# Performance work log

Measured on AMD Instinct MI355X. Metric: run time of the kernel, lower is better.

Reference implementation:

```python
import jax, jax.numpy as jnp
import numpy as np

N_SLOTS = 256
CHANNELS = 2048

def setup_inputs() -> dict:
    key = jax.random.key(0)
    k1, k2, k3, k4 = jax.random.split(key, 4)
    B, C, H, W = 32, CHANNELS, 32, 32
    x = jax.random.normal(k1, (B, C, H, W), dtype=jnp.float32)
    slot_assign = jax.random.randint(k2, (B, H, W), 0, N_SLOTS, dtype=jnp.int32)
    # slot noise tables: alpha ~ N(1, sigma1), beta ~ N(0, sigma2)
    sigma1, sigma2 = 0.1, 0.1
    alpha = 1.0 + sigma1 * jax.random.normal(k3, (N_SLOTS, CHANNELS), dtype=jnp.float32)
    beta = sigma2 * jax.random.normal(k4, (N_SLOTS, CHANNELS), dtype=jnp.float32)
    return {"x": x, "slot_assign": slot_assign, "alpha": alpha, "beta": beta}

def reference(x, slot_assign, alpha, beta):
    # Gather per-pixel (alpha, beta) rows: [B,H,W,C] -> move C to axis 1
    a = jnp.transpose(alpha[slot_assign], (0, 3, 1, 2))  # [B,C,H,W]
    b = jnp.transpose(beta[slot_assign], (0, 3, 1, 2))   # [B,C,H,W]
    return a * x + b
```

## Files before the change

### kernel.cpp

```cpp
#include <hip/hip_runtime.h>


typedef float  f4 __attribute__((ext_vector_type(4)));
typedef int    i4 __attribute__((ext_vector_type(4)));

#define CH   2048
#define HW   1024
#define NS   256
#define CPB  8
#define NCG  (CH / CPB)
#define IPB  4

__global__ __launch_bounds__(256, 4) void fa_kernel(
    const float* __restrict__ x,
    const int*   __restrict__ slot,
    const float* __restrict__ alpha,
    const float* __restrict__ beta,
    float*       __restrict__ out)
{
    __shared__ float lds_a[CPB][NS];
    __shared__ float lds_b[CPB][NS];

    const int cg = blockIdx.x & (NCG - 1);
    const int bg = blockIdx.x >> 8;
    const int b0 = bg * IPB;
    const int c0 = cg * CPB;
    const int t  = threadIdx.x;
    const int p  = t << 2;

    const f4 ar0 = *(const f4*)(alpha + (size_t)t * CH + c0);
    const f4 ar1 = *(const f4*)(alpha + (size_t)t * CH + c0 + 4);
    const f4 br0 = *(const f4*)(beta  + (size_t)t * CH + c0);
    const f4 br1 = *(const f4*)(beta  + (size_t)t * CH + c0 + 4);

#pragma unroll
    for (int k = 0; k < 4; ++k) {
        lds_a[k][t]     = ar0[k];
        lds_a[4 + k][t] = ar1[k];
        lds_b[k][t]     = br0[k];
        lds_b[4 + k][t] = br1[k];
    }

    __syncthreads();

#pragma unroll
    for (int i = 0; i < IPB; ++i) {
        const int b = b0 + i;

        const i4 s = *(const i4*)(slot + (size_t)b * HW + p);

        const size_t base = ((size_t)b * CH + c0) * HW + p;
        f4 xv[CPB];
#pragma unroll
        for (int k = 0; k < CPB; ++k)
            xv[k] = __builtin_nontemporal_load((const f4*)(x + base + (size_t)k * HW));

#pragma unroll
        for (int k = 0; k < CPB; ++k) {
            const float a0 = lds_a[k][s.x], a1 = lds_a[k][s.y],
                        a2 = lds_a[k][s.z], a3 = lds_a[k][s.w];
            const float b0v = lds_b[k][s.x], b1v = lds_b[k][s.y],
                        b2v = lds_b[k][s.z], b3v = lds_b[k][s.w];
            f4 o;
            o[0] = a0 * xv[k][0] + b0v;
            o[1] = a1 * xv[k][1] + b1v;
            o[2] = a2 * xv[k][2] + b2v;
            o[3] = a3 * xv[k][3] + b3v;
            __builtin_nontemporal_store(o, (f4*)(out + base + (size_t)k * HW));
        }
    }
}

extern "C" void kernel_launch(void* const* d_in, const int* in_sizes, int n_in,
                              void* d_out, int out_size, void* d_ws, size_t ws_size,
                              hipStream_t stream) {
    const float* x     = (const float*)d_in[0];
    const int*   slot  = (const int*)d_in[1];
    const float* alpha = (const float*)d_in[2];
    const float* beta  = (const float*)d_in[3];
    float*       out   = (float*)d_out;

    const int B = in_sizes[0] / (CH * HW);
    dim3 grid((B / IPB) * NCG);
    dim3 block(256);
    fa_kernel<<<grid, block, 0, stream>>>(x, slot, alpha, beta, out);
}
```

Before: 429.6 us.

## Double-buffer x and slot loads across images and double images per block

The kernel now prefetches the next image's slot indices and x tile into registers while the current image is being computed. The first image's loads are issued before the LDS table fill and barrier. Images per block go from 4 to 8, halving the grid and amortizing the alpha/beta table load over more work. The cost is higher register pressure from two x buffers, which could limit occupancy under launch_bounds(256,4), and fewer blocks to fill the device.

```diff
diff --git a/kernel.cpp b/kernel.cpp
--- a/kernel.cpp
+++ b/kernel.cpp
@@ -9,7 +9,7 @@
 #define NS   256
 #define CPB  8
 #define NCG  (CH / CPB)
-#define IPB  4
+#define IPB  8
 
 __global__ __launch_bounds__(256, 4) void fa_kernel(
     const float* __restrict__ x,
@@ -33,6 +33,14 @@
     const f4 br0 = *(const f4*)(beta  + (size_t)t * CH + c0);
     const f4 br1 = *(const f4*)(beta  + (size_t)t * CH + c0 + 4);
 
+    i4 s[2];
+    f4 xv[2][CPB];
+    s[0] = *(const i4*)(slot + (size_t)b0 * HW + p);
+    const size_t base0 = ((size_t)b0 * CH + c0) * HW + p;
+#pragma unroll
+    for (int k = 0; k < CPB; ++k)
+        xv[0][k] = __builtin_nontemporal_load((const f4*)(x + base0 + (size_t)k * HW));
+
 #pragma unroll
     for (int k = 0; k < 4; ++k) {
         lds_a[k][t]     = ar0[k];
@@ -45,27 +53,34 @@
 
 #pragma unroll
     for (int i = 0; i < IPB; ++i) {
-        const int b = b0 + i;
+        const int cur = i & 1;
+        const int nxt = cur ^ 1;
 
-        const i4 s = *(const i4*)(slot + (size_t)b * HW + p);
+        if (i + 1 < IPB) {
+            const int bn = b0 + i + 1;
+            s[nxt] = *(const i4*)(slot + (size_t)bn * HW + p);
+            const size_t basen = ((size_t)bn * CH + c0) * HW + p;
+#pragma unroll
+            for (int k = 0; k < CPB; ++k)
+                xv[nxt][k] = __builtin_nontemporal_load(
+                    (const f4*)(x + basen + (size_t)k * HW));
+        }
 
+        const int    b    = b0 + i;
         const size_t base = ((size_t)b * CH + c0) * HW + p;
-        f4 xv[CPB];
-#pragma unroll
-        for (int k = 0; k < CPB; ++k)
-            xv[k] = __builtin_nontemporal_load((const f4*)(x + base + (size_t)k * HW));
+        const i4     sc   = s[cur];
 
 #pragma unroll
         for (int k = 0; k < CPB; ++k) {
-            const float a0 = lds_a[k][s.x], a1 = lds_a[k][s.y],
-                        a2 = lds_a[k][s.z], a3 = lds_a[k][s.w];
-            const float b0v = lds_b[k][s.x], b1v = lds_b[k][s.y],
-                        b2v = lds_b[k][s.z], b3v = lds_b[k][s.w];
+            const float a0 = lds_a[k][sc.x], a1 = lds_a[k][sc.y],
+                        a2 = lds_a[k][sc.z], a3 = lds_a[k][sc.w];
+            const float q0 = lds_b[k][sc.x], q1 = lds_b[k][sc.y],
+                        q2 = lds_b[k][sc.z], q3 = lds_b[k][sc.w];
             f4 o;
-            o[0] = a0 * xv[k][0] + b0v;
-            o[1] = a1 * xv[k][1] + b1v;
-            o[2] = a2 * xv[k][2] + b2v;
-            o[3] = a3 * xv[k][3] + b3v;
+            o[0] = a0 * xv[cur][k][0] + q0;
+            o[1] = a1 * xv[cur][k][1] + q1;
+            o[2] = a2 * xv[cur][k][2] + q2;
+            o[3] = a3 * xv[cur][k][3] + q3;
             __builtin_nontemporal_store(o, (f4*)(out + base + (size_t)k * HW));
         }
     }
```

Measured after the change: 427.2 us. No clear change (-0.6%).
